# Kernel tuning notes

Measured on AMD Instinct MI355X. Metric: run time of the kernel, lower is better.

## Reference

```python
import jax, jax.numpy as jnp
import numpy as np

B, C, H, W = 8, 256, 48, 48
QC = C // 8                # query/key channels
MIP = max(8, C // 32)      # CoordAtt bottleneck channels
EPS = 1e-5                 # BatchNorm eps (inference, running_mean=0, running_var=1)


def _conv1x1(x, Wt, b=None):
    # 1x1 conv == channel matmul: x [b,c,h,w], Wt [o,c]
    y = jnp.einsum('bchw,oc->bohw', x, Wt)
    if b is not None:
        y = y + b[None, :, None, None]
    return y


def _bn(x, w, b):
    # inference BatchNorm with running_mean=0, running_var=1
    s = w * np.float32(1.0 / np.sqrt(1.0 + EPS))
    return x * s[None, :, None, None] + b[None, :, None, None]


def setup_inputs() -> dict:
    key = jax.random.key(0)
    ks = jax.random.split(key, 22)
    r = lambda k, sh, s=0.05: jax.random.normal(k, sh, jnp.float32) * s
    return dict(
        f1=jax.random.normal(ks[0], (B, C, H, W), jnp.float32),
        f2=jax.random.normal(ks[1], (B, C, H, W), jnp.float32),
        t1=r(ks[2], (1, C, 1, 1), 1.0),
        t2=r(ks[3], (1, C, 1, 1), 1.0),
        Wq=r(ks[4], (QC, C)), bq=r(ks[5], (QC,)),
        Wk=r(ks[6], (QC, C)), bk=r(ks[7], (QC,)),
        Wv=r(ks[8], (C, C)), bv=r(ks[9], (C,)),
        gamma=jnp.full((1,), 0.5, jnp.float32),
        ca_w1=r(ks[10], (MIP, C)), ca_b1=r(ks[11], (MIP,)),
        ca_bn_w=1.0 + r(ks[12], (MIP,)), ca_bn_b=r(ks[13], (MIP,)),
        ca_wh=r(ks[14], (C, MIP)), ca_bh=r(ks[15], (C,)),
        ca_ww=r(ks[16], (C, MIP)), ca_bw=r(ks[17], (C,)),
        fus_w=r(ks[18], (C, 2 * C)),
        fus_bn_w=1.0 + r(ks[19], (C,)), fus_bn_b=r(ks[20], (C,)),
    )


def _cross_attention(f1, f2, t1, t2, Wq, bq, Wk, bk, Wv, bv, gamma):
    b, c, h, w = f1.shape
    N = h * w
    f1e = f1 + t1
    f2e = f2 + t2

    def qkv(fe):
        q = _conv1x1(fe, Wq, bq).reshape(b, QC, N).transpose(0, 2, 1)  # [b,N,qc]
        k = _conv1x1(fe, Wk, bk).reshape(b, QC, N)                     # [b,qc,N]
        v = _conv1x1(fe, Wv, bv).reshape(b, c, N)                      # [b,c,N]
        return q, k, v

    q1, k1, v1 = qkv(f1e)
    q2, k2, v2 = qkv(f2e)

    # CrossAtt_1 = softmax(Q2 @ K1^T) applied to V1
    attn21 = jax.nn.softmax(jnp.einsum('bmq,bqn->bmn', q2, k1), axis=-1)  # [b,N,N]
    out1 = jnp.einsum('bcn,bmn->bcm', v1, attn21).reshape(b, c, h, w)
    # CrossAtt_2 = softmax(Q1 @ K2^T) applied to V2
    attn12 = jax.nn.softmax(jnp.einsum('bmq,bqn->bmn', q1, k2), axis=-1)
    out2 = jnp.einsum('bcn,bmn->bcm', v2, attn12).reshape(b, c, h, w)

    return gamma[0] * out1 + f1, gamma[0] * out2 + f2


def _coord_att(x, w1, b1, bnw, bnb, wh, bh, ww, bw):
    b, c, h, w = x.shape
    x_h = jnp.mean(x, axis=3, keepdims=True)                         # [b,c,h,1]
    x_w = jnp.mean(x, axis=2, keepdims=True).transpose(0, 1, 3, 2)   # [b,c,w,1]
    y = jnp.concatenate([x_h, x_w], axis=2)                          # [b,c,h+w,1]
    y = jax.nn.relu(_bn(_conv1x1(y, w1, b1), bnw, bnb))
    yh, yw = y[:, :, :h], y[:, :, h:]
    a_h = jax.nn.sigmoid(_conv1x1(yh, wh, bh))                       # [b,c,h,1]
    a_w = jax.nn.sigmoid(_conv1x1(yw.transpose(0, 1, 3, 2), ww, bw)) # [b,c,1,w]
    return x * a_w * a_h


def _fusion(x, Wf, bnw, bnb):
    return jax.nn.relu(_bn(_conv1x1(x, Wf), bnw, bnb))


def reference(f1, f2, t1, t2, Wq, bq, Wk, bk, Wv, bv, gamma,
              ca_w1, ca_b1, ca_bn_w, ca_bn_b, ca_wh, ca_bh, ca_ww, ca_bw,
              fus_w, fus_bn_w, fus_bn_b):
    a1, a2 = _cross_attention(f1, f2, t1, t2, Wq, bq, Wk, bk, Wv, bv, gamma)
    c1 = _coord_att(f1, ca_w1, ca_b1, ca_bn_w, ca_bn_b, ca_wh, ca_bh, ca_ww, ca_bw)
    c2 = _coord_att(f2, ca_w1, ca_b1, ca_bn_w, ca_bn_b, ca_wh, ca_bh, ca_ww, ca_bw)
    o1 = _fusion(jnp.concatenate([a1, c1], axis=1), fus_w, fus_bn_w, fus_bn_b)
    o2 = _fusion(jnp.concatenate([a2, c2], axis=1), fus_w, fus_bn_w, fus_bn_b)
    return o1, o2
```

## Files before the change

kernel.cpp:

```cpp
#include <hip/hip_runtime.h>
#include <hip/hip_bf16.h>

typedef unsigned short ushort_t;
typedef __attribute__((ext_vector_type(8))) short short8;
typedef __attribute__((ext_vector_type(4))) float floatx4;
typedef __attribute__((ext_vector_type(16))) float floatx16;
typedef __attribute__((ext_vector_type(4))) unsigned int uintx4;


__device__ __forceinline__ float bf2f(ushort_t u) {
    return __uint_as_float(((unsigned int)u) << 16);
}
__device__ __forceinline__ ushort_t f2bf(float f) {
    unsigned int x = __float_as_uint(f);
    unsigned int r = (x + 0x7fffu + ((x >> 16) & 1u)) >> 16;
    return (ushort_t)r;
}
__device__ __forceinline__ unsigned int pkbf(float a, float b) {
    __hip_bfloat162 h = __float22bfloat162_rn(float2{a, b});
    return *reinterpret_cast<unsigned int*>(&h);
}
__device__ __forceinline__ float loadIn(const void* p, size_t i, int isbf) {
    return isbf ? bf2f(((const ushort_t*)p)[i]) : ((const float*)p)[i];
}
__device__ __forceinline__ float fexp2(float x) {
#if __has_builtin(__builtin_amdgcn_exp2f)
    return __builtin_amdgcn_exp2f(x);
#else
    return exp2f(x);
#endif
}
__device__ __forceinline__ void plswap(unsigned& a, unsigned& b, int h) {
#if __has_builtin(__builtin_amdgcn_permlane32_swap)
    auto r = __builtin_amdgcn_permlane32_swap(a, b, false, false);
    a = r[0];
    b = r[1];
#else
    unsigned sa = __shfl_xor(a, 32), sb = __shfl_xor(b, 32);
    unsigned na = (h == 0) ? a : sb;
    unsigned nb = (h == 0) ? sa : b;
    a = na; b = nb;
#endif
}

#define BN_SCALE 0.9999950000374997f
#define LOG2E    1.4426950408889634f
#define ZERO16 (floatx16){0.f,0.f,0.f,0.f,0.f,0.f,0.f,0.f,0.f,0.f,0.f,0.f,0.f,0.f,0.f,0.f}

#define P_T1    0
#define P_T2    256
#define P_WQ    512
#define P_BQ    8704
#define P_WK    8768
#define P_BK    16960
#define P_WV    17024
#define P_BV    82560
#define P_GAMMA 82624
#define P_CAW1  82688
#define P_CAB1  84736
#define P_BNW   84800
#define P_BNB   84864
#define P_WH    84928
#define P_BH    86976
#define P_WW    87232
#define P_BW    89280
#define P_FUSW  89536
#define P_FBNW  220608
#define P_FBNB  220864
#define P_BQ2   221120

#define COORD_BLOCKS 16

__global__ void detect_kernel(const void* gamma, int* flag) {
    if (threadIdx.x == 0) {
        ushort_t u = ((const ushort_t*)gamma)[0];
        *flag = (u != 0) ? 1 : 0;
    }
}

__global__ __launch_bounds__(256) void convert_params(
    const void* t1, const void* t2, const void* Wq, const void* bq,
    const void* Wk, const void* bk, const void* Wv, const void* bv,
    const void* gm, const void* cw1, const void* cb1, const void* bnw,
    const void* bnb, const void* wh, const void* bh, const void* ww,
    const void* bw, const void* fw, const void* fbnw, const void* fbnb,
    const int* flagp, float* dst, ushort_t* WA, ushort_t* WF)
{
    int isbf = *flagp;
    const void* srcs[20] = {t1,t2,Wq,bq,Wk,bk,Wv,bv,gm,cw1,cb1,bnw,bnb,wh,bh,ww,bw,fw,fbnw,fbnb};
    const int   cnts[20] = {256,256,8192,32,8192,32,65536,256,1,2048,8,8,8,2048,256,2048,256,131072,256,256};
    const int   offs[20] = {P_T1,P_T2,P_WQ,P_BQ,P_WK,P_BK,P_WV,P_BV,P_GAMMA,P_CAW1,P_CAB1,
                            P_BNW,P_BNB,P_WH,P_BH,P_WW,P_BW,P_FUSW,P_FBNW,P_FBNB};
    int tid = blockIdx.x * 256 + threadIdx.x;
    int stride = gridDim.x * 256;
    #pragma unroll
    for (int sg = 0; sg < 20; sg++) {
        float* d = dst + offs[sg];
        for (int i = tid; i < cnts[sg]; i += stride) d[i] = loadIn(srcs[sg], i, isbf);
    }
    for (int i = tid; i < 81920; i += stride) {
        int o = i >> 8, c = i & 255;
        float v;
        if (o < 32)      v = loadIn(Wq, o * 256 + c, isbf);
        else if (o < 64) v = loadIn(Wk, (o - 32) * 256 + c, isbf);
        else             v = loadIn(Wv, (size_t)(o - 64) * 256 + c, isbf);
        WA[i] = f2bf(v);
    }
    for (int i = tid; i < 131072; i += stride) WF[i] = f2bf(loadIn(fw, i, isbf));
    int gw = tid >> 6, lane = tid & 63;
    if (gw < 640) {
        int side = gw / 320, o = gw % 320;
        const void* tsrc = side ? t2 : t1;
        float bias; const void* Wsrc; size_t wbase;
        if (o < 32)      { bias = loadIn(bq, o, isbf);       Wsrc = Wq; wbase = (size_t)o * 256; }
        else if (o < 64) { bias = loadIn(bk, o - 32, isbf);  Wsrc = Wk; wbase = (size_t)(o - 32) * 256; }
        else             { bias = loadIn(bv, o - 64, isbf);  Wsrc = Wv; wbase = (size_t)(o - 64) * 256; }
        float s = 0.f;
        for (int c = lane; c < 256; c += 64) s += loadIn(Wsrc, wbase + c, isbf) * loadIn(tsrc, c, isbf);
        s += __shfl_xor(s, 1);  s += __shfl_xor(s, 2);  s += __shfl_xor(s, 4);
        s += __shfl_xor(s, 8);  s += __shfl_xor(s, 16); s += __shfl_xor(s, 32);
        if (lane == 0) dst[P_BQ2 + gw] = bias + s;
    }
}

__global__ __launch_bounds__(256) void prep_qkv(
    const void* __restrict__ f1, const void* __restrict__ f2,
    const int* __restrict__ flagp,
    const ushort_t* __restrict__ WA, const float* __restrict__ P,
    ushort_t* __restrict__ fT,
    ushort_t* __restrict__ qG, ushort_t* __restrict__ kG, ushort_t* __restrict__ vG)
{
    __shared__ ushort_t xs[64][264];
    int isbf = *flagp;
    int blk = blockIdx.x;
    int nt = blk % 36, sb = blk / 36;
    int side = sb >> 3, b = sb & 7;
    int n0 = nt * 64;
    const void* f = side ? f2 : f1;
    int t = threadIdx.x;
    size_t base = ((size_t)b * 256 + t) * 2304 + n0;
    if (isbf) {
        const ushort_t* fp = (const ushort_t*)f + base;
        #pragma unroll
        for (int i = 0; i < 8; i++) {
            uint4 raw = *(const uint4*)&fp[i * 8];
            const ushort_t* rp = (const ushort_t*)&raw;
            #pragma unroll
            for (int j = 0; j < 8; j++) xs[i * 8 + j][t] = rp[j];
        }
    } else {
        const float* fp = (const float*)f + base;
        #pragma unroll
        for (int i = 0; i < 16; i++) {
            float4 raw = *(const float4*)&fp[i * 4];
            unsigned u0 = pkbf(raw.x, raw.y), u1 = pkbf(raw.z, raw.w);
            xs[i * 4 + 0][t] = (ushort_t)u0;
            xs[i * 4 + 1][t] = (ushort_t)(u0 >> 16);
            xs[i * 4 + 2][t] = (ushort_t)u1;
            xs[i * 4 + 3][t] = (ushort_t)(u1 >> 16);
        }
    }
    __syncthreads();
    #pragma unroll
    for (int i = 0; i < 8; i++) {
        int chunk = i * 256 + t;
        int row = chunk >> 5, k8 = (chunk & 31) * 8;
        *(uint4*)&fT[((size_t)sb * 2304 + n0 + row) * 256 + k8] = *(const uint4*)&xs[row][k8];
    }
    int w = t >> 6, l = t & 63, q = l >> 4, ln = l & 15;
    floatx4 acc[5][4];
    #pragma unroll
    for (int mi = 0; mi < 5; mi++)
        #pragma unroll
        for (int ns = 0; ns < 4; ns++) acc[mi][ns] = (floatx4){0.f, 0.f, 0.f, 0.f};
    #pragma unroll
    for (int ks = 0; ks < 8; ks++) {
        short8 a[5];
        #pragma unroll
        for (int mi = 0; mi < 5; mi++)
            a[mi] = *(const short8*)&WA[(size_t)(w * 80 + mi * 16 + ln) * 256 + ks * 32 + q * 8];
        #pragma unroll
        for (int ns = 0; ns < 4; ns++) {
            short8 bfr = *(const short8*)&xs[ns * 16 + ln][ks * 32 + q * 8];
            #pragma unroll
            for (int mi = 0; mi < 5; mi++)
                acc[mi][ns] = __builtin_amdgcn_mfma_f32_16x16x32_bf16(a[mi], bfr, acc[mi][ns], 0, 0, 0);
        }
    }
    const float* bp = P + P_BQ2 + side * 320;
    #pragma unroll
    for (int mi = 0; mi < 5; mi++) {
        int o0 = w * 80 + mi * 16 + q * 4;
        if (o0 >= 64) continue;
        #pragma unroll
        for (int ns = 0; ns < 4; ns++) {
            int n = n0 + ns * 16 + ln;
            if (o0 < 32) {
                uint2 pk;
                pk.x = pkbf((acc[mi][ns][0] + bp[o0]) * LOG2E, (acc[mi][ns][1] + bp[o0 + 1]) * LOG2E);
                pk.y = pkbf((acc[mi][ns][2] + bp[o0 + 2]) * LOG2E, (acc[mi][ns][3] + bp[o0 + 3]) * LOG2E);
                *(uint2*)&qG[((size_t)sb * 2304 + n) * 32 + o0] = pk;
            } else {
                uint2 pk;
                pk.x = pkbf(acc[mi][ns][0] + bp[o0], acc[mi][ns][1] + bp[o0 + 1]);
                pk.y = pkbf(acc[mi][ns][2] + bp[o0 + 2], acc[mi][ns][3] + bp[o0 + 3]);
                *(uint2*)&kG[((size_t)sb * 2304 + n) * 32 + (o0 - 32)] = pk;
            }
        }
    }
    ushort_t* vst = &xs[0][0];
    ushort_t* vgb = vG + (size_t)sb * 256 * 2304;
    int row8 = t >> 3, c8 = (t & 7) * 8;
    #pragma unroll
    for (int half = 0; half < 2; half++) {
        __syncthreads();
        int lo = 64 + half * 128;
        #pragma unroll
        for (int mi = 0; mi < 5; mi++) {
            int o0 = w * 80 + mi * 16 + q * 4;
            if (o0 < lo || o0 >= lo + 128) continue;
            int vr0 = o0 - lo;
            #pragma unroll
            for (int ns = 0; ns < 4; ns++) {
                int col = ns * 16 + ln;
                #pragma unroll
                for (int r = 0; r < 4; r++)
                    vst[(vr0 + r) * 72 + col] = f2bf(acc[mi][ns][r] + bp[o0 + r]);
            }
        }
        __syncthreads();
        #pragma unroll
        for (int pass = 0; pass < 4; pass++) {
            int row = pass * 32 + row8;
            uint4 v = *(const uint4*)&vst[row * 72 + c8];
            *(uint4*)&vgb[(size_t)(half * 128 + row) * 2304 + n0 + c8] = v;
        }
    }
}

__global__ __launch_bounds__(256) void pool_kernel(
    const ushort_t* __restrict__ fT, float* __restrict__ pools,
    float* __restrict__ lsum)
{
    int blk = blockIdx.x;
    int c = threadIdx.x;
    if (blk < 576 && c < 64) lsum[blk * 64 + c] = 0.f;
    int j = blk % 96, sb = blk / 96;
    const ushort_t* base = fT + (size_t)sb * 2304 * 256 + c;
    float s = 0.f;
    if (j < 48) {
        int h = j;
        #pragma unroll 8
        for (int w = 0; w < 48; w++) s += bf2f(base[(size_t)(h * 48 + w) * 256]);
    } else {
        int w = j - 48;
        #pragma unroll 8
        for (int h = 0; h < 48; h++) s += bf2f(base[(size_t)(h * 48 + w) * 256]);
    }
    pools[(size_t)sb * 24576 + c * 96 + j] = s * (1.f / 48.f);
}

__global__ __launch_bounds__(256) void attn_coord(
    const ushort_t* __restrict__ qG, const ushort_t* __restrict__ kG,
    const ushort_t* __restrict__ vG,
    ushort_t* __restrict__ O0, ushort_t* __restrict__ O1,
    float* __restrict__ lsum,
    const float* __restrict__ pools, const float* __restrict__ P,
    float* __restrict__ attv)
{
    __shared__ __align__(16) ushort_t vsm[4][64 * 68];
    __shared__ __align__(16) ushort_t paf[8192];

    int t = threadIdx.x;

    if (blockIdx.x < COORD_BLOCKS) {
        float* w1s = (float*)&vsm[0][0];
        float* ys  = w1s + 2048;
        int sb = blockIdx.x;
        for (int ff = t; ff < 2048; ff += 256) w1s[ff] = P[P_CAW1 + ff];
        __syncthreads();
        const float* pin = pools + (size_t)sb * 24576;
        if (t < 96) {
            float s[8];
            #pragma unroll
            for (int mp = 0; mp < 8; mp++) s[mp] = 0.f;
            for (int c = 0; c < 256; c++) {
                float p = pin[c * 96 + t];
                #pragma unroll
                for (int mp = 0; mp < 8; mp++) s[mp] += w1s[mp * 256 + c] * p;
            }
            #pragma unroll
            for (int mp = 0; mp < 8; mp++) {
                float vv = s[mp] + P[P_CAB1 + mp];
                vv = vv * (P[P_BNW + mp] * BN_SCALE) + P[P_BNB + mp];
                ys[mp * 96 + t] = fmaxf(vv, 0.f);
            }
        }
        __syncthreads();
        float* aout = attv + (size_t)sb * 24576;
        for (int ff = t; ff < 24576; ff += 256) {
            int j = ff >> 8, c = ff & 255;
            const float* W = P + ((j < 48) ? P_WH : P_WW);
            const float* B = P + ((j < 48) ? P_BH : P_BW);
            float s = B[c];
            #pragma unroll
            for (int mp = 0; mp < 8; mp++) s += W[c * 8 + mp] * ys[mp * 96 + j];
            aout[ff] = 1.f / (1.f + __expf(-s));
        }
        return;
    }

    int i = blockIdx.x - COORD_BLOCKS;
    int xcd = i & 7, slot = i >> 3;
    int dhi = (slot >= 72) ? 1 : 0;
    int db = xcd + (dhi << 3);
    int rem = slot - 72 * dhi;
    int sp = rem & 1, mt = rem >> 1;
    int qsb = db ^ 8;

    int w = t >> 6;
    int qsw = w & 1, ksw = w >> 1;
    int l = t & 63, r31 = l & 31, h = l >> 5;
    int q0 = mt * 64, c0 = w * 64;

    short8 qf0, qf1;
    {
        const ushort_t* qrow = qG + ((size_t)qsb * 2304 + q0 + qsw * 32 + r31) * 32;
        qf0 = *(const short8*)&qrow[h * 8];
        qf1 = *(const short8*)&qrow[16 + h * 8];
    }

    const ushort_t* kW = kG + ((size_t)db * 2304 + ksw * 32 + r31) * 32 + h * 8;
    const ushort_t* vbase = vG + ((size_t)db * 256 + c0) * 2304;
    ushort_t* vw = &vsm[w][0];
    int vls = (l >> 3);
    int vlc = (l & 7) * 8;

    floatx16 o[2][2];
    #pragma unroll
    for (int qs = 0; qs < 2; qs++)
        #pragma unroll
        for (int cs = 0; cs < 2; cs++) o[qs][cs] = ZERO16;
    float l_lane = 0.f;

    int nstart = sp * 1152;

#define V_LOAD(VR, N0)                                                         \
    _Pragma("unroll")                                                          \
    for (int i_ = 0; i_ < 8; i_++) {                                           \
        int r_ = i_ * 8 + vls;                                                 \
        VR[i_] = *(const uint4*)&vbase[(size_t)r_ * 2304 + (N0) + vlc];        \
    }
#define V_STORE(VR)                                                            \
    _Pragma("unroll")                                                          \
    for (int i_ = 0; i_ < 8; i_++) {                                           \
        int a_ = (i_ * 8 + vls) * 68 + vlc;                                    \
        *(uint2*)&vw[a_]     = make_uint2(VR[i_].x, VR[i_].y);                 \
        *(uint2*)&vw[a_ + 4] = make_uint2(VR[i_].z, VR[i_].w);                 \
    }

#define DO_S_PUBLISH(K0, K1, BUF)                                              \
    {                                                                          \
        floatx16 s_ = ZERO16;                                                  \
        s_ = __builtin_amdgcn_mfma_f32_32x32x16_bf16(K0, qf0, s_, 0, 0, 0);    \
        s_ = __builtin_amdgcn_mfma_f32_32x32x16_bf16(K1, qf1, s_, 0, 0, 0);    \
        float e_[16];                                                          \
        _Pragma("unroll")                                                      \
        for (int r_ = 0; r_ < 16; r_++) e_[r_] = fexp2(s_[r_]);                \
        l_lane += (((e_[0] + e_[1]) + (e_[2] + e_[3]))                         \
                 + ((e_[4] + e_[5]) + (e_[6] + e_[7])))                        \
                + (((e_[8] + e_[9]) + (e_[10] + e_[11]))                       \
                 + ((e_[12] + e_[13]) + (e_[14] + e_[15])));                   \
        unsigned wd_[8];                                                       \
        _Pragma("unroll")                                                      \
        for (int p_ = 0; p_ < 8; p_++) wd_[p_] = pkbf(e_[2 * p_], e_[2 * p_ + 1]); \
        plswap(wd_[0], wd_[2], h); plswap(wd_[1], wd_[3], h);                  \
        plswap(wd_[4], wd_[6], h); plswap(wd_[5], wd_[7], h);                  \
        uintx4 A0_ = {wd_[0], wd_[1], wd_[2], wd_[3]};                         \
        uintx4 A1_ = {wd_[4], wd_[5], wd_[6], wd_[7]};                         \
        *(uintx4*)&paf[(size_t)((((BUF) * 2 + qsw) * 4 + ksw * 2 + 0) * 64 + l) * 8] = A0_; \
        *(uintx4*)&paf[(size_t)((((BUF) * 2 + qsw) * 4 + ksw * 2 + 1) * 64 + l) * 8] = A1_; \
    }

#define DO_PV(BUF)                                                             \
    __builtin_amdgcn_s_setprio(1);                                             \
    _Pragma("unroll")                                                          \
    for (int kt = 0; kt < 4; kt++) {                                           \
        short8 af0 = *(const short8*)&paf[(size_t)((((BUF) * 2 + 0) * 4 + kt) * 64 + l) * 8]; \
        short8 af1 = *(const short8*)&paf[(size_t)((((BUF) * 2 + 1) * 4 + kt) * 64 + l) * 8]; \
        _Pragma("unroll")                                                      \
        for (int cs = 0; cs < 2; cs++) {                                       \
            int va_ = (cs * 32 + r31) * 68 + kt * 16 + h * 8;                  \
            uint2 u0_ = *(const uint2*)&vw[va_];                               \
            uint2 u1_ = *(const uint2*)&vw[va_ + 4];                           \
            uintx4 vv_ = {u0_.x, u0_.y, u1_.x, u1_.y};                         \
            short8 vf_ = *(const short8*)&vv_;                                 \
            o[0][cs] = __builtin_amdgcn_mfma_f32_32x32x16_bf16(af0, vf_, o[0][cs], 0, 0, 0); \
            o[1][cs] = __builtin_amdgcn_mfma_f32_32x32x16_bf16(af1, vf_, o[1][cs], 0, 0, 0); \
        }                                                                      \
    }                                                                          \
    __builtin_amdgcn_s_setprio(0);

    uint4 vr[8];
    V_LOAD(vr, nstart)
    {
        const ushort_t* kp = kW + (size_t)nstart * 32;
        short8 k0 = *(const short8*)&kp[0];
        short8 k1 = *(const short8*)&kp[16];
        DO_S_PUBLISH(k0, k1, 0)
    }
    V_STORE(vr)
    __syncthreads();

    for (int tile = 0; tile < 17; tile++) {
        int n0 = nstart + tile * 64;
        int buf = tile & 1;
        const ushort_t* kp = kW + (size_t)(n0 + 64) * 32;
        short8 k0n = *(const short8*)&kp[0];
        short8 k1n = *(const short8*)&kp[16];
        V_LOAD(vr, n0 + 64)
        DO_PV(buf)
        DO_S_PUBLISH(k0n, k1n, (buf ^ 1))
        V_STORE(vr)
        __syncthreads();
    }
    DO_PV(1)
#undef DO_PV
#undef DO_S_PUBLISH
#undef V_STORE
#undef V_LOAD

    float lt = l_lane + __shfl_xor(l_lane, 32);
    if (h == 0)
        atomicAdd(&lsum[(size_t)db * 2304 + q0 + qsw * 32 + r31], lt);
    ushort_t* Op = sp ? O1 : O0;
    size_t obase = ((size_t)db * 2304 + q0) * 256 + c0;
    ushort_t* ow = vw;
    int rrow8 = l >> 3, rch0 = (l & 7) * 8;
    #pragma unroll
    for (int qs = 0; qs < 2; qs++) {
        #pragma unroll
        for (int cs = 0; cs < 2; cs++) {
            #pragma unroll
            for (int r = 0; r < 16; r++) {
                int qloc = (r & 3) + 8 * (r >> 2) + 4 * h;
                ow[qloc * 72 + cs * 32 + r31] = f2bf(o[qs][cs][r]);
            }
        }
        #pragma unroll
        for (int pass = 0; pass < 4; pass++) {
            int row = pass * 8 + rrow8;
            uintx4 v = *(const uintx4*)&ow[row * 72 + rch0];
            __builtin_nontemporal_store(v, (uintx4*)&Op[obase + (size_t)(qs * 32 + row) * 256 + rch0]);
        }
    }
}

__global__ __launch_bounds__(256) void fusion_gemm(
    const ushort_t* __restrict__ O0, const ushort_t* __restrict__ O1,
    const ushort_t* __restrict__ fT, const float* __restrict__ attv,
    const float* __restrict__ lsum,
    const ushort_t* __restrict__ WF, const float* __restrict__ P,
    const int* __restrict__ flagp, void* __restrict__ dout)
{
    __shared__ ushort_t xs[64][264];
    __shared__ float sS[64];
    int isbf = *flagp;
    int blk = blockIdx.x;
    int nt = blk % 36, sb = blk / 36;
    int n0 = nt * 64;
    int t = threadIdx.x;
    int w = t >> 6, l = t & 63, q = l >> 4, ln = l & 15;
    if (t < 64) {
        sS[t] = P[P_GAMMA] / lsum[(size_t)sb * 2304 + n0 + t];
    }
    __syncthreads();
    floatx4 acc[4][4];
    #pragma unroll
    for (int ms = 0; ms < 4; ms++)
        #pragma unroll
        for (int ns = 0; ns < 4; ns++) acc[ms][ns] = (floatx4){0.f, 0.f, 0.f, 0.f};
    size_t tbase = ((size_t)sb * 2304 + n0) * 256;
    #pragma unroll
    for (int i = 0; i < 8; i++) {
        int chunk = i * 256 + t;
        int row = chunk >> 5, k8 = (chunk & 31) * 8;
        size_t idx = tbase + (size_t)row * 256 + k8;
        uintx4 u0 = __builtin_nontemporal_load((const uintx4*)&O0[idx]);
        uintx4 u1 = __builtin_nontemporal_load((const uintx4*)&O1[idx]);
        uint4 uf = *(const uint4*)&fT[idx];
        const ushort_t* a0 = (const ushort_t*)&u0;
        const ushort_t* a1 = (const ushort_t*)&u1;
        const ushort_t* ff = (const ushort_t*)&uf;
        float s = sS[row];
        float v[8];
        #pragma unroll
        for (int j = 0; j < 8; j++) v[j] = (bf2f(a0[j]) + bf2f(a1[j])) * s + bf2f(ff[j]);
        uint4 pk;
        pk.x = pkbf(v[0], v[1]); pk.y = pkbf(v[2], v[3]);
        pk.z = pkbf(v[4], v[5]); pk.w = pkbf(v[6], v[7]);
        *(uint4*)&xs[row][k8] = pk;
    }
    __syncthreads();
    #pragma unroll
    for (int ks = 0; ks < 8; ks++) {
        short8 a[4];
        #pragma unroll
        for (int ms = 0; ms < 4; ms++)
            a[ms] = *(const short8*)&WF[(size_t)(w * 64 + ms * 16 + ln) * 512 + ks * 32 + q * 8];
        #pragma unroll
        for (int ns = 0; ns < 4; ns++) {
            short8 bfr = *(const short8*)&xs[ns * 16 + ln][ks * 32 + q * 8];
            #pragma unroll
            for (int ms = 0; ms < 4; ms++)
                acc[ms][ns] = __builtin_amdgcn_mfma_f32_16x16x32_bf16(a[ms], bfr, acc[ms][ns], 0, 0, 0);
        }
    }
    __syncthreads();
    const float* av = attv + (size_t)sb * 24576;
    #pragma unroll
    for (int i = 0; i < 8; i++) {
        int chunk = i * 256 + t;
        int row = chunk >> 5, k8 = (chunk & 31) * 8;
        int n = n0 + row;
        int h = n / 48, ww2 = n - h * 48;
        size_t idx = tbase + (size_t)row * 256 + k8;
        uint4 uf = *(const uint4*)&fT[idx];
        const ushort_t* ff = (const ushort_t*)&uf;
        float ah[8], aw[8];
        *(float4*)&ah[0] = *(const float4*)&av[h * 256 + k8];
        *(float4*)&ah[4] = *(const float4*)&av[h * 256 + k8 + 4];
        *(float4*)&aw[0] = *(const float4*)&av[(48 + ww2) * 256 + k8];
        *(float4*)&aw[4] = *(const float4*)&av[(48 + ww2) * 256 + k8 + 4];
        float v[8];
        #pragma unroll
        for (int j = 0; j < 8; j++) v[j] = bf2f(ff[j]) * ah[j] * aw[j];
        uint4 pk;
        pk.x = pkbf(v[0], v[1]); pk.y = pkbf(v[2], v[3]);
        pk.z = pkbf(v[4], v[5]); pk.w = pkbf(v[6], v[7]);
        *(uint4*)&xs[row][k8] = pk;
    }
    __syncthreads();
    #pragma unroll
    for (int ks = 0; ks < 8; ks++) {
        short8 a[4];
        #pragma unroll
        for (int ms = 0; ms < 4; ms++)
            a[ms] = *(const short8*)&WF[(size_t)(w * 64 + ms * 16 + ln) * 512 + 256 + ks * 32 + q * 8];
        #pragma unroll
        for (int ns = 0; ns < 4; ns++) {
            short8 bfr = *(const short8*)&xs[ns * 16 + ln][ks * 32 + q * 8];
            #pragma unroll
            for (int ms = 0; ms < 4; ms++)
                acc[ms][ns] = __builtin_amdgcn_mfma_f32_16x16x32_bf16(a[ms], bfr, acc[ms][ns], 0, 0, 0);
        }
    }
    #pragma unroll
    for (int ms = 0; ms < 4; ms++) {
        int o0 = w * 64 + ms * 16 + q * 4;
        float bw[4], bb[4];
        #pragma unroll
        for (int r = 0; r < 4; r++) {
            bw[r] = P[P_FBNW + o0 + r] * BN_SCALE;
            bb[r] = P[P_FBNB + o0 + r];
        }
        #pragma unroll
        for (int ns = 0; ns < 4; ns++) {
            int n = n0 + ns * 16 + ln;
            #pragma unroll
            for (int r = 0; r < 4; r++) {
                float v = acc[ms][ns][r] * bw[r] + bb[r];
                v = (v < 0.f) ? 0.f : v;
                size_t oidx = (size_t)sb * 589824 + (size_t)(o0 + r) * 2304 + n;
                if (isbf) ((ushort_t*)dout)[oidx] = f2bf(v);
                else      ((float*)dout)[oidx] = v;
            }
        }
    }
}

extern "C" void kernel_launch(void* const* d_in, const int* in_sizes, int n_in,
                              void* d_out, int out_size, void* d_ws, size_t ws_size,
                              hipStream_t stream) {
    const void* f1 = d_in[0]; const void* f2 = d_in[1];

    char* ws = (char*)d_ws;
    int*      flag  = (int*)(ws + 0);
    float*    P     = (float*)(ws + 1024);
    ushort_t* WA    = (ushort_t*)(ws + 917504);
    ushort_t* WF    = (ushort_t*)(ws + 1081344);
    ushort_t* fT    = (ushort_t*)(ws + 1343488);
    ushort_t* qG    = (ushort_t*)(ws + 20217856);
    ushort_t* kG    = (ushort_t*)(ws + 22577152);
    ushort_t* vG    = (ushort_t*)(ws + 24936448);
    ushort_t* O0    = (ushort_t*)(ws + 43810816);
    float*    pools = (float*)(ws + 62685184);
    float*    attv  = (float*)(ws + 64258048);
    ushort_t* O1    = (ushort_t*)(ws + 65830912);
    float*    lsum  = (float*)(ws + 917504);

    detect_kernel<<<dim3(1), dim3(64), 0, stream>>>(d_in[10], flag);
    convert_params<<<dim3(160), dim3(256), 0, stream>>>(
        d_in[2], d_in[3], d_in[4], d_in[5], d_in[6], d_in[7], d_in[8], d_in[9],
        d_in[10], d_in[11], d_in[12], d_in[13], d_in[14], d_in[15], d_in[16],
        d_in[17], d_in[18], d_in[19], d_in[20], d_in[21], flag, P, WA, WF);
    prep_qkv<<<dim3(576), dim3(256), 0, stream>>>(f1, f2, flag, WA, P, fT, qG, kG, vG);
    pool_kernel<<<dim3(1536), dim3(256), 0, stream>>>(fT, pools, lsum);
    attn_coord<<<dim3(1168), dim3(256), 0, stream>>>(qG, kG, vG, O0, O1, lsum, pools, P, attv);
    fusion_gemm<<<dim3(576), dim3(256), 0, stream>>>(
        O0, O1, fT, attv, lsum, WF, P, flag, d_out);
}
```

Before: 302.8 us.

## Drop split-N attention, remove partial output buffer and detect kernel

Each attention block now walks the full key range (35+1 tiles) instead of half, so the grid goes from 1168 to 592 blocks. This removes the second partial output buffer O1, the atomic row-sum accumulation and the lsum zeroing in the pool kernel; row sums are reduced in shared memory and written directly. The separate dtype-detect kernel is removed and each kernel reads gamma inline. The trade-off is fewer blocks for the attention stage, each doing longer serial work, against less memory traffic in fusion and one fewer launch.

```diff
diff --git a/kernel.cpp b/kernel.cpp
--- a/kernel.cpp
+++ b/kernel.cpp
@@ -22,6 +22,9 @@
 }
 __device__ __forceinline__ float loadIn(const void* p, size_t i, int isbf) {
     return isbf ? bf2f(((const ushort_t*)p)[i]) : ((const float*)p)[i];
+}
+__device__ __forceinline__ int probe_bf(const void* gm) {
+    return (((const ushort_t*)gm)[0] != 0) ? 1 : 0;
 }
 __device__ __forceinline__ float fexp2(float x) {
 #if __has_builtin(__builtin_amdgcn_exp2f)
@@ -71,22 +74,15 @@
 
 #define COORD_BLOCKS 16
 
-__global__ void detect_kernel(const void* gamma, int* flag) {
-    if (threadIdx.x == 0) {
-        ushort_t u = ((const ushort_t*)gamma)[0];
-        *flag = (u != 0) ? 1 : 0;
-    }
-}
-
 __global__ __launch_bounds__(256) void convert_params(
     const void* t1, const void* t2, const void* Wq, const void* bq,
     const void* Wk, const void* bk, const void* Wv, const void* bv,
     const void* gm, const void* cw1, const void* cb1, const void* bnw,
     const void* bnb, const void* wh, const void* bh, const void* ww,
     const void* bw, const void* fw, const void* fbnw, const void* fbnb,
-    const int* flagp, float* dst, ushort_t* WA, ushort_t* WF)
+    float* dst, ushort_t* WA, ushort_t* WF)
 {
-    int isbf = *flagp;
+    int isbf = probe_bf(gm);
     const void* srcs[20] = {t1,t2,Wq,bq,Wk,bk,Wv,bv,gm,cw1,cb1,bnw,bnb,wh,bh,ww,bw,fw,fbnw,fbnb};
     const int   cnts[20] = {256,256,8192,32,8192,32,65536,256,1,2048,8,8,8,2048,256,2048,256,131072,256,256};
     const int   offs[20] = {P_T1,P_T2,P_WQ,P_BQ,P_WK,P_BK,P_WV,P_BV,P_GAMMA,P_CAW1,P_CAB1,
@@ -125,13 +121,13 @@
 
 __global__ __launch_bounds__(256) void prep_qkv(
     const void* __restrict__ f1, const void* __restrict__ f2,
-    const int* __restrict__ flagp,
+    const void* __restrict__ gm,
     const ushort_t* __restrict__ WA, const float* __restrict__ P,
     ushort_t* __restrict__ fT,
     ushort_t* __restrict__ qG, ushort_t* __restrict__ kG, ushort_t* __restrict__ vG)
 {
     __shared__ ushort_t xs[64][264];
-    int isbf = *flagp;
+    int isbf = probe_bf(gm);
     int blk = blockIdx.x;
     int nt = blk % 36, sb = blk / 36;
     int side = sb >> 3, b = sb & 7;
@@ -239,12 +235,10 @@
 }
 
 __global__ __launch_bounds__(256) void pool_kernel(
-    const ushort_t* __restrict__ fT, float* __restrict__ pools,
-    float* __restrict__ lsum)
+    const ushort_t* __restrict__ fT, float* __restrict__ pools)
 {
     int blk = blockIdx.x;
     int c = threadIdx.x;
-    if (blk < 576 && c < 64) lsum[blk * 64 + c] = 0.f;
     int j = blk % 96, sb = blk / 96;
     const ushort_t* base = fT + (size_t)sb * 2304 * 256 + c;
     float s = 0.f;
@@ -263,13 +257,14 @@
 __global__ __launch_bounds__(256) void attn_coord(
     const ushort_t* __restrict__ qG, const ushort_t* __restrict__ kG,
     const ushort_t* __restrict__ vG,
-    ushort_t* __restrict__ O0, ushort_t* __restrict__ O1,
+    ushort_t* __restrict__ O0,
     float* __restrict__ lsum,
     const float* __restrict__ pools, const float* __restrict__ P,
     float* __restrict__ attv)
 {
     __shared__ __align__(16) ushort_t vsm[4][64 * 68];
     __shared__ __align__(16) ushort_t paf[8192];
+    __shared__ float lred[4][32];
 
     int t = threadIdx.x;
 
@@ -312,10 +307,9 @@
 
     int i = blockIdx.x - COORD_BLOCKS;
     int xcd = i & 7, slot = i >> 3;
-    int dhi = (slot >= 72) ? 1 : 0;
+    int dhi = (slot >= 36) ? 1 : 0;
     int db = xcd + (dhi << 3);
-    int rem = slot - 72 * dhi;
-    int sp = rem & 1, mt = rem >> 1;
+    int mt = slot - 36 * dhi;
     int qsb = db ^ 8;
 
     int w = t >> 6;
@@ -342,8 +336,6 @@
         #pragma unroll
         for (int cs = 0; cs < 2; cs++) o[qs][cs] = ZERO16;
     float l_lane = 0.f;
-
-    int nstart = sp * 1152;
 
 #define V_LOAD(VR, N0)                                                         \
     _Pragma("unroll")                                                          \
@@ -382,7 +374,7 @@
         *(uintx4*)&paf[(size_t)((((BUF) * 2 + qsw) * 4 + ksw * 2 + 1) * 64 + l) * 8] = A1_; \
     }
 
-#define DO_PV(BUF)                                                             \
+#define DO_PV(BUF, N0)                                                         \
     __builtin_amdgcn_s_setprio(1);                                             \
     _Pragma("unroll")                                                          \
     for (int kt = 0; kt < 4; kt++) {                                           \
@@ -402,9 +394,9 @@
     __builtin_amdgcn_s_setprio(0);
 
     uint4 vr[8];
-    V_LOAD(vr, nstart)
+    V_LOAD(vr, 0)
     {
-        const ushort_t* kp = kW + (size_t)nstart * 32;
+        const ushort_t* kp = kW;
         short8 k0 = *(const short8*)&kp[0];
         short8 k1 = *(const short8*)&kp[16];
         DO_S_PUBLISH(k0, k1, 0)
@@ -412,28 +404,26 @@
     V_STORE(vr)
     __syncthreads();
 
-    for (int tile = 0; tile < 17; tile++) {
-        int n0 = nstart + tile * 64;
+    for (int tile = 0; tile < 35; tile++) {
+        int n0 = tile * 64;
         int buf = tile & 1;
         const ushort_t* kp = kW + (size_t)(n0 + 64) * 32;
         short8 k0n = *(const short8*)&kp[0];
         short8 k1n = *(const short8*)&kp[16];
         V_LOAD(vr, n0 + 64)
-        DO_PV(buf)
+        DO_PV(buf, n0)
         DO_S_PUBLISH(k0n, k1n, (buf ^ 1))
         V_STORE(vr)
         __syncthreads();
     }
-    DO_PV(1)
+    DO_PV(1, 2240)
 #undef DO_PV
 #undef DO_S_PUBLISH
 #undef V_STORE
 #undef V_LOAD
 
     float lt = l_lane + __shfl_xor(l_lane, 32);
-    if (h == 0)
-        atomicAdd(&lsum[(size_t)db * 2304 + q0 + qsw * 32 + r31], lt);
-    ushort_t* Op = sp ? O1 : O0;
+    lred[w][r31] = lt;
     size_t obase = ((size_t)db * 2304 + q0) * 256 + c0;
     ushort_t* ow = vw;
     int rrow8 = l >> 3, rch0 = (l & 7) * 8;
@@ -451,21 +441,26 @@
         for (int pass = 0; pass < 4; pass++) {
             int row = pass * 8 + rrow8;
             uintx4 v = *(const uintx4*)&ow[row * 72 + rch0];
-            __builtin_nontemporal_store(v, (uintx4*)&Op[obase + (size_t)(qs * 32 + row) * 256 + rch0]);
-        }
+            __builtin_nontemporal_store(v, (uintx4*)&O0[obase + (size_t)(qs * 32 + row) * 256 + rch0]);
+        }
+    }
+    __syncthreads();
+    if (t < 64) {
+        int qs = t >> 5, r = t & 31;
+        lsum[(size_t)db * 2304 + q0 + t] = lred[qs][r] + lred[qs + 2][r];
     }
 }
 
 __global__ __launch_bounds__(256) void fusion_gemm(
-    const ushort_t* __restrict__ O0, const ushort_t* __restrict__ O1,
+    const ushort_t* __restrict__ O0,
     const ushort_t* __restrict__ fT, const float* __restrict__ attv,
     const float* __restrict__ lsum,
     const ushort_t* __restrict__ WF, const float* __restrict__ P,
-    const int* __restrict__ flagp, void* __restrict__ dout)
+    const void* __restrict__ gm, void* __restrict__ dout)
 {
     __shared__ ushort_t xs[64][264];
     __shared__ float sS[64];
-    int isbf = *flagp;
+    int isbf = probe_bf(gm);
     int blk = blockIdx.x;
     int nt = blk % 36, sb = blk / 36;
     int n0 = nt * 64;
@@ -487,15 +482,13 @@
         int row = chunk >> 5, k8 = (chunk & 31) * 8;
         size_t idx = tbase + (size_t)row * 256 + k8;
         uintx4 u0 = __builtin_nontemporal_load((const uintx4*)&O0[idx]);
-        uintx4 u1 = __builtin_nontemporal_load((const uintx4*)&O1[idx]);
         uint4 uf = *(const uint4*)&fT[idx];
         const ushort_t* a0 = (const ushort_t*)&u0;
-        const ushort_t* a1 = (const ushort_t*)&u1;
         const ushort_t* ff = (const ushort_t*)&uf;
         float s = sS[row];
         float v[8];
         #pragma unroll
-        for (int j = 0; j < 8; j++) v[j] = (bf2f(a0[j]) + bf2f(a1[j])) * s + bf2f(ff[j]);
+        for (int j = 0; j < 8; j++) v[j] = bf2f(a0[j]) * s + bf2f(ff[j]);
         uint4 pk;
         pk.x = pkbf(v[0], v[1]); pk.y = pkbf(v[2], v[3]);
         pk.z = pkbf(v[4], v[5]); pk.w = pkbf(v[6], v[7]);
@@ -583,9 +576,9 @@
                               void* d_out, int out_size, void* d_ws, size_t ws_size,
                               hipStream_t stream) {
     const void* f1 = d_in[0]; const void* f2 = d_in[1];
+    const void* gm = d_in[10];
 
     char* ws = (char*)d_ws;
-    int*      flag  = (int*)(ws + 0);
     float*    P     = (float*)(ws + 1024);
     ushort_t* WA    = (ushort_t*)(ws + 917504);
     ushort_t* WF    = (ushort_t*)(ws + 1081344);
@@ -596,17 +589,15 @@
     ushort_t* O0    = (ushort_t*)(ws + 43810816);
     float*    pools = (float*)(ws + 62685184);
     float*    attv  = (float*)(ws + 64258048);
-    ushort_t* O1    = (ushort_t*)(ws + 65830912);
     float*    lsum  = (float*)(ws + 917504);
 
-    detect_kernel<<<dim3(1), dim3(64), 0, stream>>>(d_in[10], flag);
     convert_params<<<dim3(160), dim3(256), 0, stream>>>(
         d_in[2], d_in[3], d_in[4], d_in[5], d_in[6], d_in[7], d_in[8], d_in[9],
         d_in[10], d_in[11], d_in[12], d_in[13], d_in[14], d_in[15], d_in[16],
-        d_in[17], d_in[18], d_in[19], d_in[20], d_in[21], flag, P, WA, WF);
-    prep_qkv<<<dim3(576), dim3(256), 0, stream>>>(f1, f2, flag, WA, P, fT, qG, kG, vG);
-    pool_kernel<<<dim3(1536), dim3(256), 0, stream>>>(fT, pools, lsum);
-    attn_coord<<<dim3(1168), dim3(256), 0, stream>>>(qG, kG, vG, O0, O1, lsum, pools, P, attv);
+        d_in[17], d_in[18], d_in[19], d_in[20], d_in[21], P, WA, WF);
+    prep_qkv<<<dim3(576), dim3(256), 0, stream>>>(f1, f2, gm, WA, P, fT, qG, kG, vG);
+    pool_kernel<<<dim3(1536), dim3(256), 0, stream>>>(fT, pools);
+    attn_coord<<<dim3(592), dim3(256), 0, stream>>>(qG, kG, vG, O0, lsum, pools, P, attv);
     fusion_gemm<<<dim3(576), dim3(256), 0, stream>>>(
-        O0, O1, fT, attv, lsum, WF, P, flag, d_out);
-}
+        O0, fT, attv, lsum, WF, P, gm, d_out);
+}
```

Measured after the change: 317.4 us. 4.8% more time.
